# Optimization experiments

Hardware: AMD Instinct MI355X
Metric: run time of the kernel (lower is better)

The kernel has to match this reference:

```python
import jax, jax.numpy as jnp
import numpy as np

ALPHA = 0.2   # LeakyReLU negative slope
NEG = -1e9    # mask value for non-edges


def setup_inputs() -> dict:
    key = jax.random.key(0)
    ks = jax.random.split(key, 8)
    N, Din, F, H, Dout = 4096, 512, 64, 8, 16
    adj = (jax.random.uniform(ks[0], (N, N)) < 0.01).astype(jnp.float32)
    adjacency = jnp.maximum(adj, jnp.eye(N, dtype=jnp.float32))
    X = jax.random.normal(ks[1], (N, Din), jnp.float32)
    s = lambda k, shape, fan: jax.random.normal(k, shape, jnp.float32) / np.float32(np.sqrt(fan))
    W = s(ks[2], (H, Din, F), Din)        # per-head projection, stacked
    a1 = s(ks[3], (H, F), F)              # attention vector, source half
    a2 = s(ks[4], (H, F), F)              # attention vector, target half
    Wo = s(ks[5], (H * F, Dout), H * F)   # output-layer projection
    ao1 = s(ks[6], (Dout,), Dout)
    ao2 = s(ks[7], (Dout,), Dout)
    return dict(adjacency=adjacency, X=X, W=W, a1=a1, a2=a2, Wo=Wo, ao1=ao1, ao2=ao2)


def reference(adjacency, X, W, a1, a2, Wo, ao1, ao2):
    # dropout is identity (eval mode / p=0)
    mask = adjacency > 0
    N = X.shape[0]
    # --- multi-head attention layers (concat=True -> ELU) ---
    Wh = jnp.einsum('nd,hdf->hnf', X, W)                      # [H, N, F]
    f1 = jnp.einsum('hnf,hf->hn', Wh, a1)                     # [H, N]
    f2 = jnp.einsum('hnf,hf->hn', Wh, a2)                     # [H, N]
    e = jax.nn.leaky_relu(f1[:, :, None] + f2[:, None, :], ALPHA)  # [H, N, N]
    att = jax.nn.softmax(jnp.where(mask[None], e, NEG), axis=-1)
    heads = jax.nn.elu(jnp.einsum('hnm,hmf->hnf', att, Wh))   # [H, N, F]
    cat = jnp.transpose(heads, (1, 0, 2)).reshape(N, -1)      # [N, H*F]
    # --- output attention layer (concat=False -> no ELU) ---
    Who = cat @ Wo                                            # [N, Dout]
    eo = jax.nn.leaky_relu((Who @ ao1)[:, None] + (Who @ ao2)[None, :], ALPHA)
    atto = jax.nn.softmax(jnp.where(mask, eo, NEG), axis=-1)  # [N, N]
    return atto @ Who                                         # [N, Dout]
```

## Files before the change

kernel.cpp:

```cpp
#include <hip/hip_runtime.h>
#include <hip/hip_bf16.h>

#define N_NODES 4096
#define DIN     512
#define FDIM    64
#define NHEADS  8
#define DOUT    16
#define MAXN    512

typedef __attribute__((ext_vector_type(8))) short bf16x8;
typedef __attribute__((ext_vector_type(4))) float f32x4;

static __device__ __forceinline__ float us2f(unsigned short u) {
    union { unsigned int i; float f; } cv; cv.i = ((unsigned int)u) << 16; return cv.f;
}
static __device__ __forceinline__ unsigned short f2us(float v) {
    __hip_bfloat16 b = __float2bfloat16(v);
    return *(const unsigned short*)&b;
}
static __device__ __forceinline__ int is_f32(const void* adj) {
    return (((const unsigned short*)adj)[0] == 0) ? 1 : 0;
}

__global__ __launch_bounds__(256) void prep_nbr_kernel(
    const void* __restrict__ adj, const void* __restrict__ X, const void* __restrict__ W,
    const void* __restrict__ a1, const void* __restrict__ a2, const void* __restrict__ Wo,
    const void* __restrict__ ao1, const void* __restrict__ ao2,
    unsigned short* __restrict__ Xb, unsigned short* __restrict__ Wt,
    float* __restrict__ Woc,
    float* __restrict__ a1c, float* __restrict__ a2c,
    float* __restrict__ ao1c, float* __restrict__ ao2c,
    int* __restrict__ cnt, int* __restrict__ nbr)
{
    const int f32 = is_f32(adj);
    if (blockIdx.x >= 1024) {
        const int n = blockIdx.x - 1024;
        __shared__ int c;
        if (threadIdx.x == 0) c = 0;
        __syncthreads();
        if (f32) {
            const uint4* row = (const uint4*)((const unsigned int*)adj + (size_t)n * N_NODES);
            for (int q = threadIdx.x; q < N_NODES / 4; q += 256) {
                uint4 v = row[q];
                int base = q * 4;
                if (v.x) { int p = atomicAdd(&c, 1); if (p < MAXN) nbr[(size_t)n * MAXN + p] = base + 0; }
                if (v.y) { int p = atomicAdd(&c, 1); if (p < MAXN) nbr[(size_t)n * MAXN + p] = base + 1; }
                if (v.z) { int p = atomicAdd(&c, 1); if (p < MAXN) nbr[(size_t)n * MAXN + p] = base + 2; }
                if (v.w) { int p = atomicAdd(&c, 1); if (p < MAXN) nbr[(size_t)n * MAXN + p] = base + 3; }
            }
        } else {
            const ushort4* row = (const ushort4*)((const unsigned short*)adj + (size_t)n * N_NODES);
            for (int q = threadIdx.x; q < N_NODES / 4; q += 256) {
                ushort4 v = row[q];
                int base = q * 4;
                if (v.x) { int p = atomicAdd(&c, 1); if (p < MAXN) nbr[(size_t)n * MAXN + p] = base + 0; }
                if (v.y) { int p = atomicAdd(&c, 1); if (p < MAXN) nbr[(size_t)n * MAXN + p] = base + 1; }
                if (v.z) { int p = atomicAdd(&c, 1); if (p < MAXN) nbr[(size_t)n * MAXN + p] = base + 2; }
                if (v.w) { int p = atomicAdd(&c, 1); if (p < MAXN) nbr[(size_t)n * MAXN + p] = base + 3; }
            }
        }
        __syncthreads();
        if (threadIdx.x == 0) cnt[n] = (c < MAXN) ? c : MAXN;
        return;
    }
    const int i0 = blockIdx.x * 256 + threadIdx.x;
    const int T = 1024 * 256;
    for (int i = i0; i < N_NODES * DIN; i += T) {
        float v = f32 ? ((const float*)X)[i] : us2f(((const unsigned short*)X)[i]);
        Xb[i] = f2us(v);
    }
    for (int i = i0; i < NHEADS * DIN * FDIM; i += T) {
        int hh = i >> 15, rem = i & 32767, d = rem >> 6, f = rem & 63;
        float v = f32 ? ((const float*)W)[i] : us2f(((const unsigned short*)W)[i]);
        Wt[((size_t)(hh * FDIM + f)) * DIN + d] = f2us(v);
    }
    if (i0 < DIN * DOUT) {
        float v = f32 ? ((const float*)Wo)[i0] : us2f(((const unsigned short*)Wo)[i0]);
        Woc[i0] = v;
    }
    if (i0 < 512) {
        a1c[i0] = f32 ? ((const float*)a1)[i0] : us2f(((const unsigned short*)a1)[i0]);
        a2c[i0] = f32 ? ((const float*)a2)[i0] : us2f(((const unsigned short*)a2)[i0]);
    }
    if (i0 < 16) {
        ao1c[i0] = f32 ? ((const float*)ao1)[i0] : us2f(((const unsigned short*)ao1)[i0]);
        ao2c[i0] = f32 ? ((const float*)ao2)[i0] : us2f(((const unsigned short*)ao2)[i0]);
    }
}

__global__ __launch_bounds__(256) void wh_f12_kernel(
    const unsigned short* __restrict__ Xb, const unsigned short* __restrict__ Wt,
    const float* __restrict__ a1c, const float* __restrict__ a2c,
    unsigned short* __restrict__ Whb, float* __restrict__ f1, float* __restrict__ f2)
{
    const int h  = blockIdx.x;
    const int bm = blockIdx.y;
    const int w    = threadIdx.x >> 6;
    const int lane = threadIdx.x & 63;
    const int quad = lane >> 4;
    const int l16  = lane & 15;
    const int node = bm * 64 + w * 16 + l16;

    f32x4 acc[4];
#pragma unroll
    for (int j = 0; j < 4; ++j) acc[j] = (f32x4){0.f, 0.f, 0.f, 0.f};

    const unsigned short* xp = Xb + (size_t)node * DIN + quad * 8;
    const unsigned short* wp = Wt + (size_t)h * FDIM * DIN + quad * 8;
#pragma unroll 4
    for (int k0 = 0; k0 < DIN; k0 += 32) {
        bf16x8 b = *(const bf16x8*)(xp + k0);
#pragma unroll
        for (int j = 0; j < 4; ++j) {
            bf16x8 a = *(const bf16x8*)(wp + (size_t)(j * 16 + l16) * DIN + k0);
            acc[j] = __builtin_amdgcn_mfma_f32_16x16x32_bf16(a, b, acc[j], 0, 0, 0);
        }
    }
    float p1 = 0.f, p2 = 0.f;
#pragma unroll
    for (int j = 0; j < 4; ++j) {
        const int fbase = j * 16 + quad * 4;
        ushort4 st;
        st.x = f2us(acc[j][0]); st.y = f2us(acc[j][1]);
        st.z = f2us(acc[j][2]); st.w = f2us(acc[j][3]);
        *(ushort4*)&Whb[((size_t)node * NHEADS + h) * FDIM + fbase] = st;
#pragma unroll
        for (int rr = 0; rr < 4; ++rr) {
            p1 += acc[j][rr] * a1c[h * FDIM + fbase + rr];
            p2 += acc[j][rr] * a2c[h * FDIM + fbase + rr];
        }
    }
    p1 += __shfl_xor(p1, 16); p1 += __shfl_xor(p1, 32);
    p2 += __shfl_xor(p2, 16); p2 += __shfl_xor(p2, 32);
    if (quad == 0) {
        f1[h * N_NODES + node] = p1;
        f2[h * N_NODES + node] = p2;
    }
}

__global__ __launch_bounds__(256) void attn1_kernel(
    const unsigned short* __restrict__ Whb,
    const float* __restrict__ f1, const float* __restrict__ f2,
    const float* __restrict__ Woc,
    const float* __restrict__ ao1c, const float* __restrict__ ao2c,
    const int* __restrict__ cnt, const int* __restrict__ nbr,
    float* __restrict__ Who, float* __restrict__ g1, float* __restrict__ g2)
{
    const int n   = blockIdx.x;
    const int tid = threadIdx.x;
    const int wv  = tid >> 6;
    const int lane = tid & 63;
    const int hh = lane >> 3;

    __shared__ int   sh_m[MAXN];
    __shared__ float sh_red[3][64][9];
    __shared__ float sh_ml[4][NHEADS][2];
    __shared__ float cat_sh[512];
    __shared__ float sh_p[16 * 17];

    const int c0 = cnt[n];
    const int c = (c0 < MAXN) ? c0 : MAXN;
    for (int k = tid; k < c; k += 256) sh_m[k] = nbr[(size_t)n * MAXN + k];
    __syncthreads();

    const float f1v = f1[hh * N_NODES + n];
    float m_run = -1e30f, l_run = 0.f;
    float acc8[8];
#pragma unroll
    for (int e = 0; e < 8; ++e) acc8[e] = 0.f;
    const uint4* wb = (const uint4*)Whb;
#pragma unroll 2
    for (int kb = 0; kb < c; kb += 4) {
        const int k = kb + wv;
        if (k < c) {
            const int mm = sh_m[k];
            uint4 v = wb[(size_t)mm * 64 + lane];
            float s = f1v + f2[hh * N_NODES + mm];
            s = (s >= 0.f) ? s : 0.2f * s;
            if (s > m_run + 8.f) {
                float scale = __expf(m_run - s);
                l_run *= scale;
#pragma unroll
                for (int e = 0; e < 8; ++e) acc8[e] *= scale;
                m_run = s;
            }
            float wgt = __expf(s - m_run);
            l_run += wgt;
            acc8[0] += wgt * us2f((unsigned short)(v.x & 0xFFFFu));
            acc8[1] += wgt * us2f((unsigned short)(v.x >> 16));
            acc8[2] += wgt * us2f((unsigned short)(v.y & 0xFFFFu));
            acc8[3] += wgt * us2f((unsigned short)(v.y >> 16));
            acc8[4] += wgt * us2f((unsigned short)(v.z & 0xFFFFu));
            acc8[5] += wgt * us2f((unsigned short)(v.z >> 16));
            acc8[6] += wgt * us2f((unsigned short)(v.w & 0xFFFFu));
            acc8[7] += wgt * us2f((unsigned short)(v.w >> 16));
        }
    }
    if (wv) {
#pragma unroll
        for (int e = 0; e < 8; ++e) sh_red[wv - 1][lane][e] = acc8[e];
    }
    if ((lane & 7) == 0) {
        sh_ml[wv][hh][0] = m_run;
        sh_ml[wv][hh][1] = l_run;
    }
    __syncthreads();
    if (wv == 0) {
        float m1 = sh_ml[1][hh][0], m2 = sh_ml[2][hh][0], m3 = sh_ml[3][hh][0];
        float M = fmaxf(fmaxf(m_run, m1), fmaxf(m2, m3));
        float c0f = __expf(m_run - M), c1f = __expf(m1 - M);
        float c2f = __expf(m2 - M),  c3f = __expf(m3 - M);
        float denom = l_run * c0f + sh_ml[1][hh][1] * c1f
                    + sh_ml[2][hh][1] * c2f + sh_ml[3][hh][1] * c3f;
        const float inv = (denom > 0.f) ? 1.f / denom : 0.f;
#pragma unroll
        for (int e = 0; e < 8; ++e) {
            float s = acc8[e] * c0f + sh_red[0][lane][e] * c1f
                    + sh_red[1][lane][e] * c2f + sh_red[2][lane][e] * c3f;
            s *= inv;
            s = (s > 0.f) ? s : expm1f(s);
            cat_sh[lane * 8 + e] = s;
        }
    }
    __syncthreads();

    {
        const int j = tid & 15, ch = tid >> 4;
        float s = 0.f;
#pragma unroll
        for (int d = 0; d < 32; ++d)
            s += cat_sh[ch * 32 + d] * Woc[(ch * 32 + d) * DOUT + j];
        sh_p[ch * 17 + j] = s;
    }
    __syncthreads();
    if (tid < 16) {
        float s = 0.f;
#pragma unroll
        for (int ch = 0; ch < 16; ++ch) s += sh_p[ch * 17 + tid];
        Who[n * DOUT + tid] = s;
        float p1 = s * ao1c[tid];
        float p2 = s * ao2c[tid];
#pragma unroll
        for (int off = 8; off; off >>= 1) {
            p1 += __shfl_xor(p1, off);
            p2 += __shfl_xor(p2, off);
        }
        if (tid == 0) { g1[n] = p1; g2[n] = p2; }
    }
}

__global__ __launch_bounds__(64) void attn2_kernel(
    const void* __restrict__ adj,
    const float* __restrict__ Who,
    const float* __restrict__ g1, const float* __restrict__ g2,
    const int* __restrict__ cnt, const int* __restrict__ nbr,
    void* __restrict__ out)
{
    const int n = blockIdx.x;
    const int lane = threadIdx.x;
    const int quad = lane >> 4, l16 = lane & 15;
    __shared__ float sh_s[MAXN];
    __shared__ int sh_m[MAXN];
    const int c0 = cnt[n];
    const int c = (c0 < MAXN) ? c0 : MAXN;
    for (int k = lane; k < c; k += 64) sh_m[k] = nbr[(size_t)n * MAXN + k];
    __syncthreads();
    const float gn = g1[n];
    float mx = -1e30f;
    for (int k = lane; k < c; k += 64) {
        float s = gn + g2[sh_m[k]];
        s = (s >= 0.f) ? s : 0.2f * s;
        sh_s[k] = s;
        mx = fmaxf(mx, s);
    }
#pragma unroll
    for (int off = 32; off; off >>= 1) mx = fmaxf(mx, __shfl_xor(mx, off));
    __syncthreads();
    float sum = 0.f;
    for (int k = lane; k < c; k += 64) {
        float e = __expf(sh_s[k] - mx);
        sh_s[k] = e;
        sum += e;
    }
#pragma unroll
    for (int off = 32; off; off >>= 1) sum += __shfl_xor(sum, off);
    __syncthreads();
    const float inv = (sum > 0.f) ? 1.f / sum : 0.f;
    float accv = 0.f;
#pragma unroll 4
    for (int k = quad; k < c; k += 4)
        accv += sh_s[k] * Who[sh_m[k] * DOUT + l16];
    accv += __shfl_xor(accv, 16);
    accv += __shfl_xor(accv, 32);
    if (quad == 0) {
        float v = accv * inv;
        if (is_f32(adj)) ((float*)out)[n * DOUT + l16] = v;
        else             ((unsigned short*)out)[n * DOUT + l16] = f2us(v);
    }
}

__global__ void wsfail_kernel(float* __restrict__ out)
{
    if (threadIdx.x == 0) out[0] = 129.f;
}

extern "C" void kernel_launch(void* const* d_in, const int* in_sizes, int n_in,
                              void* d_out, int out_size, void* d_ws, size_t ws_size,
                              hipStream_t stream)
{
    const void* adj = d_in[0];
    const void* X   = d_in[1];
    const void* W   = d_in[2];
    const void* a1  = d_in[3];
    const void* a2  = d_in[4];
    const void* Wo  = d_in[5];
    const void* ao1 = d_in[6];
    const void* ao2 = d_in[7];

    const size_t NEEDED = 22000000;
    if (ws_size < NEEDED) { wsfail_kernel<<<1, 64, 0, stream>>>((float*)d_out); return; }

    int*   cnt  = (int*)d_ws;
    int*   nbr  = cnt + 4096;
    float* a1c  = (float*)(nbr + 2097152);
    float* a2c  = a1c + 512;
    float* ao1c = a2c + 512;
    float* ao2c = ao1c + 16;
    float* f1   = ao2c + 16;
    float* f2   = f1 + 32768;
    float* Who  = f2 + 32768;
    float* g1   = Who + 65536;
    float* g2   = g1 + 4096;
    float* Woc  = g2 + 4096;
    unsigned short* Whb = (unsigned short*)(Woc + 8192);
    unsigned short* Xb  = Whb + 2097152;
    unsigned short* Wt  = Xb + 2097152;

    prep_nbr_kernel<<<1024 + N_NODES, 256, 0, stream>>>(
        adj, X, W, a1, a2, Wo, ao1, ao2,
        Xb, Wt, Woc, a1c, a2c, ao1c, ao2c, cnt, nbr);
    wh_f12_kernel<<<dim3(NHEADS, N_NODES / 64), 256, 0, stream>>>(
        Xb, Wt, a1c, a2c, Whb, f1, f2);
    attn1_kernel<<<N_NODES, 256, 0, stream>>>(
        Whb, f1, f2, Woc, ao1c, ao2c, cnt, nbr, Who, g1, g2);
    attn2_kernel<<<N_NODES, 64, 0, stream>>>(adj, Who, g1, g2, cnt, nbr, d_out);
}
```

Measured before the change: 163.3 us.

## Fuse adjacency scan with projection GEMM and convert X to bf16 inline

The adjacency neighbor scan moves out of the prep kernel into a combined kernel that interleaves scan blocks with projection-GEMM blocks (2 scan blocks per 1 GEMM block), so the memory-bound scan and the MFMA work overlap on the device. The separate X-to-bf16 conversion pass and its workspace buffer are removed, and X is converted to bf16 in registers inside the GEMM. The GEMM tile shrinks to 16 nodes per block with split-K across 4 waves and a shared-memory reduction. This adds cross-wave reduction overhead and re-reads W for each smaller tile.

Result: slower. 168.2 us (+3.0%).

```diff
diff --git a/kernel.cpp b/kernel.cpp
--- a/kernel.cpp
+++ b/kernel.cpp
@@ -22,53 +22,17 @@
     return (((const unsigned short*)adj)[0] == 0) ? 1 : 0;
 }
 
-__global__ __launch_bounds__(256) void prep_nbr_kernel(
-    const void* __restrict__ adj, const void* __restrict__ X, const void* __restrict__ W,
+__global__ __launch_bounds__(256) void prep_kernel(
+    const void* __restrict__ adj, const void* __restrict__ W,
     const void* __restrict__ a1, const void* __restrict__ a2, const void* __restrict__ Wo,
     const void* __restrict__ ao1, const void* __restrict__ ao2,
-    unsigned short* __restrict__ Xb, unsigned short* __restrict__ Wt,
-    float* __restrict__ Woc,
+    unsigned short* __restrict__ Wt, float* __restrict__ Woc,
     float* __restrict__ a1c, float* __restrict__ a2c,
-    float* __restrict__ ao1c, float* __restrict__ ao2c,
-    int* __restrict__ cnt, int* __restrict__ nbr)
+    float* __restrict__ ao1c, float* __restrict__ ao2c)
 {
     const int f32 = is_f32(adj);
-    if (blockIdx.x >= 1024) {
-        const int n = blockIdx.x - 1024;
-        __shared__ int c;
-        if (threadIdx.x == 0) c = 0;
-        __syncthreads();
-        if (f32) {
-            const uint4* row = (const uint4*)((const unsigned int*)adj + (size_t)n * N_NODES);
-            for (int q = threadIdx.x; q < N_NODES / 4; q += 256) {
-                uint4 v = row[q];
-                int base = q * 4;
-                if (v.x) { int p = atomicAdd(&c, 1); if (p < MAXN) nbr[(size_t)n * MAXN + p] = base + 0; }
-                if (v.y) { int p = atomicAdd(&c, 1); if (p < MAXN) nbr[(size_t)n * MAXN + p] = base + 1; }
-                if (v.z) { int p = atomicAdd(&c, 1); if (p < MAXN) nbr[(size_t)n * MAXN + p] = base + 2; }
-                if (v.w) { int p = atomicAdd(&c, 1); if (p < MAXN) nbr[(size_t)n * MAXN + p] = base + 3; }
-            }
-        } else {
-            const ushort4* row = (const ushort4*)((const unsigned short*)adj + (size_t)n * N_NODES);
-            for (int q = threadIdx.x; q < N_NODES / 4; q += 256) {
-                ushort4 v = row[q];
-                int base = q * 4;
-                if (v.x) { int p = atomicAdd(&c, 1); if (p < MAXN) nbr[(size_t)n * MAXN + p] = base + 0; }
-                if (v.y) { int p = atomicAdd(&c, 1); if (p < MAXN) nbr[(size_t)n * MAXN + p] = base + 1; }
-                if (v.z) { int p = atomicAdd(&c, 1); if (p < MAXN) nbr[(size_t)n * MAXN + p] = base + 2; }
-                if (v.w) { int p = atomicAdd(&c, 1); if (p < MAXN) nbr[(size_t)n * MAXN + p] = base + 3; }
-            }
-        }
-        __syncthreads();
-        if (threadIdx.x == 0) cnt[n] = (c < MAXN) ? c : MAXN;
-        return;
-    }
     const int i0 = blockIdx.x * 256 + threadIdx.x;
-    const int T = 1024 * 256;
-    for (int i = i0; i < N_NODES * DIN; i += T) {
-        float v = f32 ? ((const float*)X)[i] : us2f(((const unsigned short*)X)[i]);
-        Xb[i] = f2us(v);
-    }
+    const int T = 256 * 256;
     for (int i = i0; i < NHEADS * DIN * FDIM; i += T) {
         int hh = i >> 15, rem = i & 32767, d = rem >> 6, f = rem & 63;
         float v = f32 ? ((const float*)W)[i] : us2f(((const unsigned short*)W)[i]);
@@ -88,53 +52,128 @@
     }
 }
 
-__global__ __launch_bounds__(256) void wh_f12_kernel(
-    const unsigned short* __restrict__ Xb, const unsigned short* __restrict__ Wt,
+__global__ __launch_bounds__(256) void scan_wh_kernel(
+    const void* __restrict__ adj, const void* __restrict__ X,
+    const unsigned short* __restrict__ Wt,
     const float* __restrict__ a1c, const float* __restrict__ a2c,
+    int* __restrict__ cnt, int* __restrict__ nbr,
     unsigned short* __restrict__ Whb, float* __restrict__ f1, float* __restrict__ f2)
 {
-    const int h  = blockIdx.x;
-    const int bm = blockIdx.y;
-    const int w    = threadIdx.x >> 6;
-    const int lane = threadIdx.x & 63;
+    const int b   = blockIdx.x;
+    const int r3m = b % 3;
+    const int tid = threadIdx.x;
+    const int f32 = is_f32(adj);
+
+    __shared__ int   sh_c;
+    __shared__ float red[3][16][68];
+
+    if (r3m < 2) {
+        const int n = (b / 3) * 2 + r3m;
+        if (tid == 0) sh_c = 0;
+        __syncthreads();
+        if (f32) {
+            const uint4* row = (const uint4*)((const unsigned int*)adj + (size_t)n * N_NODES);
+#pragma unroll 4
+            for (int q = tid; q < N_NODES / 4; q += 256) {
+                uint4 v = row[q];
+                int base = q * 4;
+                if (v.x) { int p = atomicAdd(&sh_c, 1); if (p < MAXN) nbr[(size_t)n * MAXN + p] = base + 0; }
+                if (v.y) { int p = atomicAdd(&sh_c, 1); if (p < MAXN) nbr[(size_t)n * MAXN + p] = base + 1; }
+                if (v.z) { int p = atomicAdd(&sh_c, 1); if (p < MAXN) nbr[(size_t)n * MAXN + p] = base + 2; }
+                if (v.w) { int p = atomicAdd(&sh_c, 1); if (p < MAXN) nbr[(size_t)n * MAXN + p] = base + 3; }
+            }
+        } else {
+            const ushort4* row = (const ushort4*)((const unsigned short*)adj + (size_t)n * N_NODES);
+#pragma unroll 4
+            for (int q = tid; q < N_NODES / 4; q += 256) {
+                ushort4 v = row[q];
+                int base = q * 4;
+                if (v.x) { int p = atomicAdd(&sh_c, 1); if (p < MAXN) nbr[(size_t)n * MAXN + p] = base + 0; }
+                if (v.y) { int p = atomicAdd(&sh_c, 1); if (p < MAXN) nbr[(size_t)n * MAXN + p] = base + 1; }
+                if (v.z) { int p = atomicAdd(&sh_c, 1); if (p < MAXN) nbr[(size_t)n * MAXN + p] = base + 2; }
+                if (v.w) { int p = atomicAdd(&sh_c, 1); if (p < MAXN) nbr[(size_t)n * MAXN + p] = base + 3; }
+            }
+        }
+        __syncthreads();
+        if (tid == 0) cnt[n] = (sh_c < MAXN) ? sh_c : MAXN;
+        return;
+    }
+
+    const int tile = b / 3;
+    const int nt   = tile >> 3;
+    const int h    = tile & 7;
+    const int w    = tid >> 6;
+    const int lane = tid & 63;
     const int quad = lane >> 4;
     const int l16  = lane & 15;
-    const int node = bm * 64 + w * 16 + l16;
+    const int node = nt * 16 + l16;
+    const int kbase = w * 128 + quad * 8;
 
     f32x4 acc[4];
 #pragma unroll
     for (int j = 0; j < 4; ++j) acc[j] = (f32x4){0.f, 0.f, 0.f, 0.f};
 
-    const unsigned short* xp = Xb + (size_t)node * DIN + quad * 8;
-    const unsigned short* wp = Wt + (size_t)h * FDIM * DIN + quad * 8;
-#pragma unroll 4
-    for (int k0 = 0; k0 < DIN; k0 += 32) {
-        bf16x8 b = *(const bf16x8*)(xp + k0);
+    const unsigned short* wp = Wt + (size_t)h * FDIM * DIN + kbase;
+    if (f32) {
+        const float* xp = (const float*)X + (size_t)node * DIN + kbase;
+#pragma unroll
+        for (int ks = 0; ks < 4; ++ks) {
+            float4 xa = *(const float4*)(xp + ks * 32);
+            float4 xb = *(const float4*)(xp + ks * 32 + 4);
+            bf16x8 xf;
+            xf[0] = (short)f2us(xa.x); xf[1] = (short)f2us(xa.y);
+            xf[2] = (short)f2us(xa.z); xf[3] = (short)f2us(xa.w);
+            xf[4] = (short)f2us(xb.x); xf[5] = (short)f2us(xb.y);
+            xf[6] = (short)f2us(xb.z); xf[7] = (short)f2us(xb.w);
+#pragma unroll
+            for (int j = 0; j < 4; ++j) {
+                bf16x8 wf = *(const bf16x8*)(wp + (size_t)(j * 16 + l16) * DIN + ks * 32);
+                acc[j] = __builtin_amdgcn_mfma_f32_16x16x32_bf16(wf, xf, acc[j], 0, 0, 0);
+            }
+        }
+    } else {
+        const unsigned short* xp = (const unsigned short*)X + (size_t)node * DIN + kbase;
+#pragma unroll
+        for (int ks = 0; ks < 4; ++ks) {
+            bf16x8 xf = *(const bf16x8*)(xp + ks * 32);
+#pragma unroll
+            for (int j = 0; j < 4; ++j) {
+                bf16x8 wf = *(const bf16x8*)(wp + (size_t)(j * 16 + l16) * DIN + ks * 32);
+                acc[j] = __builtin_amdgcn_mfma_f32_16x16x32_bf16(wf, xf, acc[j], 0, 0, 0);
+            }
+        }
+    }
+
+    if (w) {
+#pragma unroll
+        for (int j = 0; j < 4; ++j)
+            *(f32x4*)&red[w - 1][l16][j * 16 + quad * 4] = acc[j];
+    }
+    __syncthreads();
+    if (w == 0) {
+        float p1 = 0.f, p2 = 0.f;
 #pragma unroll
         for (int j = 0; j < 4; ++j) {
-            bf16x8 a = *(const bf16x8*)(wp + (size_t)(j * 16 + l16) * DIN + k0);
-            acc[j] = __builtin_amdgcn_mfma_f32_16x16x32_bf16(a, b, acc[j], 0, 0, 0);
-        }
-    }
-    float p1 = 0.f, p2 = 0.f;
-#pragma unroll
-    for (int j = 0; j < 4; ++j) {
-        const int fbase = j * 16 + quad * 4;
-        ushort4 st;
-        st.x = f2us(acc[j][0]); st.y = f2us(acc[j][1]);
-        st.z = f2us(acc[j][2]); st.w = f2us(acc[j][3]);
-        *(ushort4*)&Whb[((size_t)node * NHEADS + h) * FDIM + fbase] = st;
-#pragma unroll
-        for (int rr = 0; rr < 4; ++rr) {
-            p1 += acc[j][rr] * a1c[h * FDIM + fbase + rr];
-            p2 += acc[j][rr] * a2c[h * FDIM + fbase + rr];
-        }
-    }
-    p1 += __shfl_xor(p1, 16); p1 += __shfl_xor(p1, 32);
-    p2 += __shfl_xor(p2, 16); p2 += __shfl_xor(p2, 32);
-    if (quad == 0) {
-        f1[h * N_NODES + node] = p1;
-        f2[h * N_NODES + node] = p2;
+            const int fbase = j * 16 + quad * 4;
+            f32x4 s = acc[j];
+#pragma unroll
+            for (int p = 0; p < 3; ++p) s += *(const f32x4*)&red[p][l16][fbase];
+            ushort4 st;
+            st.x = f2us(s[0]); st.y = f2us(s[1]);
+            st.z = f2us(s[2]); st.w = f2us(s[3]);
+            *(ushort4*)&Whb[((size_t)node * NHEADS + h) * FDIM + fbase] = st;
+#pragma unroll
+            for (int rr = 0; rr < 4; ++rr) {
+                p1 += s[rr] * a1c[h * FDIM + fbase + rr];
+                p2 += s[rr] * a2c[h * FDIM + fbase + rr];
+            }
+        }
+        p1 += __shfl_xor(p1, 16); p1 += __shfl_xor(p1, 32);
+        p2 += __shfl_xor(p2, 16); p2 += __shfl_xor(p2, 32);
+        if (quad == 0) {
+            f1[h * N_NODES + node] = p1;
+            f2[h * N_NODES + node] = p2;
+        }
     }
 }
 
@@ -333,14 +372,12 @@
     float* g2   = g1 + 4096;
     float* Woc  = g2 + 4096;
     unsigned short* Whb = (unsigned short*)(Woc + 8192);
-    unsigned short* Xb  = Whb + 2097152;
-    unsigned short* Wt  = Xb + 2097152;
-
-    prep_nbr_kernel<<<1024 + N_NODES, 256, 0, stream>>>(
-        adj, X, W, a1, a2, Wo, ao1, ao2,
-        Xb, Wt, Woc, a1c, a2c, ao1c, ao2c, cnt, nbr);
-    wh_f12_kernel<<<dim3(NHEADS, N_NODES / 64), 256, 0, stream>>>(
-        Xb, Wt, a1c, a2c, Whb, f1, f2);
+    unsigned short* Wt  = Whb + 2097152;
+
+    prep_kernel<<<256, 256, 0, stream>>>(
+        adj, W, a1, a2, Wo, ao1, ao2, Wt, Woc, a1c, a2c, ao1c, ao2c);
+    scan_wh_kernel<<<6144, 256, 0, stream>>>(
+        adj, X, Wt, a1c, a2c, cnt, nbr, Whb, f1, f2);
     attn1_kernel<<<N_NODES, 256, 0, stream>>>(
         Whb, f1, f2, Woc, ao1c, ao2c, cnt, nbr, Who, g1, g2);
     attn2_kernel<<<N_NODES, 64, 0, stream>>>(adj, Who, g1, g2, cnt, nbr, d_out);
```
